# Kernel tuning notes

Hardware: AMD Instinct MI355X
Metric: run time of the kernel (lower is better)

The kernel has to match this reference:

```python
import jax, jax.numpy as jnp
import numpy as np

# dims (see shape_source)
N = 100000          # num_ent
E = 400000          # num edges
B = 2048            # batch of (sub, rel) queries
INIT_DIM = 100
UFD = 100           # user_fe_dim
ENT_DIM = INIT_DIM + 3 * UFD   # feature_method='concat' -> 400
H = 2               # attention heads
D = 64              # per-head dim
GCN = H * D         # gcn_dim = embed_dim = 128 (gcn_layer == 1)
NUM_REL = 50
NR2 = 2 * NUM_REL


def setup_inputs() -> dict:
    key = jax.random.key(0)
    ks = jax.random.split(key, 17)
    inp = {}
    # constructor / forward int tensors
    inp["edge_index"] = jax.random.randint(ks[0], (2, E), 0, N, dtype=jnp.int32)
    inp["edge_type"] = jax.random.randint(ks[1], (E,), 0, NR2, dtype=jnp.int32)
    inp["edge_type_p"] = jax.random.randint(ks[2], (E,), 0, NR2, dtype=jnp.int32)
    inp["ent_feature"] = jax.random.randint(ks[3], (N, 3), 0, 3, dtype=jnp.int32)
    inp["sub"] = jax.random.randint(ks[4], (B,), 0, N, dtype=jnp.int32)
    inp["rel"] = jax.random.randint(ks[5], (B,), 0, NR2, dtype=jnp.int32)
    inp["relp"] = jax.random.randint(ks[6], (B,), 0, NR2, dtype=jnp.int32)
    # learned parameters
    s = 0.02
    inp["id_embed"] = jax.random.normal(ks[7], (N, INIT_DIM), jnp.float32) * s
    inp["gender_tab"] = jax.random.normal(ks[8], (3, UFD), jnp.float32) * s
    inp["age_tab"] = jax.random.normal(ks[9], (9, UFD), jnp.float32) * s
    inp["level_tab"] = jax.random.normal(ks[10], (11, UFD), jnp.float32) * s
    inp["init_rel"] = jax.random.normal(ks[11], (NR2, ENT_DIM), jnp.float32) * s
    inp["W"] = jax.random.normal(ks[12], (ENT_DIM, H * D), jnp.float32) * 0.05
    inp["Wr"] = jax.random.normal(ks[13], (ENT_DIM, H * D), jnp.float32) * 0.05
    inp["att_src"] = jax.random.normal(ks[14], (H, D), jnp.float32) * 0.05
    inp["att_dst"] = jax.random.normal(ks[15], (H, D), jnp.float32) * 0.05
    inp["Wrel"] = jax.random.normal(ks[16], (ENT_DIM, GCN), jnp.float32) * 0.05
    return inp


def _segment_softmax(logits, seg, num_segments):
    # logits: [E, H], seg: [E] destination node ids
    m = jax.ops.segment_max(logits, seg, num_segments=num_segments)
    ex = jnp.exp(logits - m[seg])
    den = jax.ops.segment_sum(ex, seg, num_segments=num_segments)
    return ex / (den[seg] + 1e-16)


def _rghat_conv(x, rel_emb, edge_index, edge_type, W, Wr, att_src, att_dst, Wrel):
    # relational multi-head graph attention (RGHATConv)
    n = x.shape[0]
    h = (x @ W).reshape(n, H, D)                       # [N,H,D] projected nodes
    r_proj = (rel_emb @ Wr).reshape(-1, H, D)          # [R,H,D]
    src, dst = edge_index[0], edge_index[1]
    msg = h[src] + r_proj[edge_type]                   # [E,H,D] edge messages
    logits = jax.nn.leaky_relu(
        jnp.sum(msg * att_src, axis=-1) + jnp.sum(h[dst] * att_dst, axis=-1),
        negative_slope=0.2,
    )                                                  # [E,H]
    alpha = _segment_softmax(logits, dst, n)           # per-destination softmax
    out = jax.ops.segment_sum(alpha[..., None] * msg, dst, num_segments=n)
    out = jnp.tanh(out.reshape(n, H * D))              # [N,GCN]
    r_out = rel_emb @ Wrel                             # [R,GCN]
    return out, r_out


def reference(edge_index, edge_type, edge_type_p, ent_feature, sub, rel, relp,
              id_embed, gender_tab, age_tab, level_tab, init_rel,
              W, Wr, att_src, att_dst, Wrel):
    # feature_method == 'concat': gather per-node feature embeddings and concat
    x1 = gender_tab[ent_feature[:, 0]]
    x2 = age_tab[ent_feature[:, 1]]
    x3 = level_tab[ent_feature[:, 2]]
    init_embed = jnp.concatenate([id_embed, x1, x2, x3], axis=1)  # [N, ENT_DIM]
    # single conv layer (gcn_layer == 1); dropouts are identity in eval
    x, r = _rghat_conv(init_embed, init_rel, edge_index, edge_type,
                       W, Wr, att_src, att_dst, Wrel)
    sub_emb = x[sub]                                   # index_select gather
    # add_parent_rel == False -> r returned whole (relp unused)
    return (sub_emb, r, x)
```

## Files before the change

kernel.cpp:

```cpp
#include <hip/hip_runtime.h>
#include <hip/hip_bf16.h>
#include <hip/hip_fp16.h>

#define N_NODES 100000
#define E_EDGES 400000
#define B_SUB 2048
#define INIT_DIM 100
#define UFD 100
#define ENT_DIM 400
#define GCN 128
#define NR2 100
#define KPAD 416
#define NCH 13
#define CAP 64

typedef __attribute__((ext_vector_type(8))) short shortx8;
typedef __attribute__((ext_vector_type(4))) float floatx4;

#define OUT_R_OFF ((long)B_SUB * GCN)
#define OUT_X_OFF ((long)(B_SUB + NR2) * GCN)

__device__ __forceinline__ unsigned short f2b(float f) {
    unsigned u = __float_as_uint(f);
    u += 0x7fffu + ((u >> 16) & 1u);
    return (unsigned short)(u >> 16);
}
__device__ __forceinline__ unsigned pk2(float x, float y) {
    return (unsigned)f2b(x) | ((unsigned)f2b(y) << 16);
}
__device__ __forceinline__ float blo(unsigned u) { return __uint_as_float(u << 16); }
__device__ __forceinline__ float bhi(unsigned u) { return __uint_as_float(u & 0xFFFF0000u); }

__global__ void wt_kernel(const float* __restrict__ W, unsigned short* __restrict__ Wt,
                          int* __restrict__ cursor) {
    int idx = blockIdx.x * 256 + threadIdx.x;
    if (idx < GCN * KPAD) {
        int n = idx & 127, k = idx >> 7;
        unsigned short o = 0;
        if (k < ENT_DIM) o = f2b(W[(long)k * GCN + n]);
        Wt[(long)n * KPAD + k] = o;
    }
    if (idx < N_NODES) cursor[idx] = 0;
}

__global__ void rel_kernel(const float* __restrict__ init_rel, const float* __restrict__ Wr,
                           const float* __restrict__ Wrel, const float* __restrict__ att_src,
                           unsigned* __restrict__ rp_b, float* __restrict__ rproj_att,
                           float* __restrict__ out_r) {
    int rel = blockIdx.x;
    int tx = threadIdx.x;
    __shared__ float rl[ENT_DIM];
    __shared__ float accbuf[128];
    for (int k = tx; k < ENT_DIM; k += 128) rl[k] = init_rel[(long)rel * ENT_DIM + k];
    __syncthreads();
    float acc1 = 0.f, acc2 = 0.f;
    for (int k = 0; k < ENT_DIM; ++k) {
        float v = rl[k];
        acc1 += v * Wr[(long)k * GCN + tx];
        acc2 += v * Wrel[(long)k * GCN + tx];
    }
    out_r[rel * GCN + tx] = acc2;
    accbuf[tx] = acc1;
    int head = tx >> 6, d = tx & 63;
    float v = acc1 * att_src[head * 64 + d];
    for (int off = 32; off > 0; off >>= 1) v += __shfl_down(v, off, 64);
    if (d == 0) rproj_att[rel * 2 + head] = v;
    __syncthreads();
    if (tx < 64) rp_b[rel * 64 + tx] = pk2(accbuf[tx], accbuf[tx + 64]);
}

__global__ __launch_bounds__(512) void hgemm_kernel(
        const float* __restrict__ id_embed, const float* __restrict__ gtab,
        const float* __restrict__ atab, const float* __restrict__ ltab,
        const int* __restrict__ ent_feature, const unsigned short* __restrict__ Wt,
        const float* __restrict__ att_src, const float* __restrict__ att_dst,
        unsigned* __restrict__ h_b, float* __restrict__ hsrc_att, float* __restrict__ hdst_att) {
    __shared__ __align__(16) unsigned short Bs[GCN * KPAD];
    __shared__ float attS[GCN], attD[GCN];
    int t = threadIdx.x;
    if (t < GCN) { attS[t] = att_src[t]; attD[t] = att_dst[t]; }
    int w = t >> 6, lane = t & 63, quad = lane >> 4, l16 = lane & 15;
    int n0 = blockIdx.x * 128;
    int nrow = n0 + w * 16 + l16;
    int nclamp = nrow < N_NODES ? nrow : N_NODES - 1;
    int f0 = ent_feature[nclamp * 3];
    int f1 = ent_feature[nclamp * 3 + 1];
    int f2 = ent_feature[nclamp * 3 + 2];
    const float* pid = id_embed + (long)nclamp * INIT_DIM;
    const float* pg = gtab + f0 * UFD;
    const float* pa = atab + f1 * UFD;
    const float* pl = ltab + f2 * UFD;

    float4 va[NCH], vb[NCH];
#pragma unroll
    for (int ch = 0; ch < NCH; ++ch) {
        int kg = ch * 32 + quad * 8;
        const float* p0;
        if (kg < 100)      p0 = pid + kg;
        else if (kg < 200) p0 = pg + kg - 100;
        else if (kg < 300) p0 = pa + kg - 200;
        else if (kg < 400) p0 = pl + kg - 300;
        else               p0 = pid;
        va[ch] = *(const float4*)p0;
        int k4 = kg + 4;
        const float* p1;
        if (k4 < 100)      p1 = pid + k4;
        else if (k4 < 200) p1 = pg + k4 - 100;
        else if (k4 < 300) p1 = pa + k4 - 200;
        else if (k4 < 400) p1 = pl + k4 - 300;
        else               p1 = pid;
        vb[ch] = *(const float4*)p1;
    }

    {
        const char* gsrc = (const char*)Wt;
        char* lbase = (char*)Bs;
#pragma unroll
        for (int i = 0; i < NCH; ++i) {
            int off = i * 8192 + w * 1024;
            __builtin_amdgcn_global_load_lds(
                (const __attribute__((address_space(1))) unsigned int*)(gsrc + off + lane * 16),
                (__attribute__((address_space(3))) unsigned int*)(lbase + off), 16, 0, 0);
        }
    }

    shortx8 aF[NCH];
#pragma unroll
    for (int ch = 0; ch < NCH; ++ch) {
        uint4 u;
        u.x = pk2(va[ch].x, va[ch].y);
        u.y = pk2(va[ch].z, va[ch].w);
        u.z = pk2(vb[ch].x, vb[ch].y);
        u.w = pk2(vb[ch].z, vb[ch].w);
        aF[ch] = *(shortx8*)&u;
    }
    floatx4 acc[8];
#pragma unroll
    for (int c = 0; c < 8; ++c) acc[c] = (floatx4){0.f, 0.f, 0.f, 0.f};

    __syncthreads();

    const unsigned short* bp = &Bs[l16 * KPAD + quad * 8];
#pragma unroll
    for (int ch = 0; ch < NCH; ++ch) {
#pragma unroll
        for (int c = 0; c < 8; ++c) {
            shortx8 b = *(const shortx8*)&bp[c * 16 * KPAD + ch * 32];
            acc[c] = __builtin_amdgcn_mfma_f32_16x16x32_bf16(aF[ch], b, acc[c], 0, 0, 0);
        }
    }

    int baseRow = n0 + w * 16 + quad * 4;
#pragma unroll
    for (int i = 0; i < 4; ++i) {
        int node = baseRow + i;
        bool ok = node < N_NODES;
#pragma unroll
        for (int c = 0; c < 4; ++c)
            if (ok) h_b[(long)node * 64 + c * 16 + l16] = pk2(acc[c][i], acc[c + 4][i]);
        float s0 = 0.f, s1 = 0.f, d0 = 0.f, d1 = 0.f;
#pragma unroll
        for (int c = 0; c < 8; ++c) {
            float v = acc[c][i];
            float as_ = attS[c * 16 + l16], ad_ = attD[c * 16 + l16];
            if (c < 4) { s0 += v * as_; d0 += v * ad_; }
            else       { s1 += v * as_; d1 += v * ad_; }
        }
#pragma unroll
        for (int m = 1; m < 16; m <<= 1) {
            s0 += __shfl_xor(s0, m, 64);
            s1 += __shfl_xor(s1, m, 64);
            d0 += __shfl_xor(d0, m, 64);
            d1 += __shfl_xor(d1, m, 64);
        }
        if (ok && l16 == 0) {
            hsrc_att[node * 2] = s0; hsrc_att[node * 2 + 1] = s1;
            hdst_att[node * 2] = d0; hdst_att[node * 2 + 1] = d1;
        }
    }
}

__global__ void fill_kernel(const int* __restrict__ edge_index, const int* __restrict__ edge_type,
                            int* __restrict__ cursor,
                            const float2* __restrict__ hsrc2, const float2* __restrict__ rpa2,
                            const float2* __restrict__ hdst2,
                            uint2* __restrict__ ebuf) {
    int e = blockIdx.x * blockDim.x + threadIdx.x;
    if (e >= E_EDGES) return;
    int src = edge_index[e];
    int dst = edge_index[E_EDGES + e];
    int et = edge_type[e];
    float2 hs = hsrc2[src];
    float2 ra = rpa2[et];
    float2 hd = hdst2[dst];
    float x0 = hs.x + ra.x + hd.x;
    float x1 = hs.y + ra.y + hd.y;
    x0 = x0 > 0.f ? x0 : 0.2f * x0;
    x1 = x1 > 0.f ? x1 : 0.2f * x1;
    __half2 hh = __floats2half2_rn(__expf(x0), __expf(x1));
    union { __half2 h; unsigned u; } cv; cv.h = hh;
    int pos = atomicAdd(&cursor[dst], 1);
    if (pos < CAP)
        ebuf[(long)dst * CAP + pos] = make_uint2(((unsigned)et << 17) | (unsigned)src, cv.u);
}

__global__ __launch_bounds__(256) void agg_kernel(
        const int* __restrict__ cursor, const uint2* __restrict__ ebuf,
        const unsigned* __restrict__ h_b, const unsigned* __restrict__ rp_b,
        float* __restrict__ out_x) {
    int w = threadIdx.x >> 6, l = threadIdx.x & 63;
    int dst = blockIdx.x * 4 + w;
    int cnt = cursor[dst];
    if (cnt > CAP) cnt = CAP;
    const uint2* base = ebuf + (long)dst * CAP;
    float acc0 = 0.f, acc1 = 0.f, den0 = 0.f, den1 = 0.f;
    int j = 0;
    for (; j + 3 < cnt; j += 4) {
        uint2 v0 = base[j], v1 = base[j + 1], v2 = base[j + 2], v3 = base[j + 3];
        union { __half2 h; unsigned u; } c0, c1, c2, c3;
        c0.u = v0.y; c1.u = v1.y; c2.u = v2.y; c3.u = v3.y;
        float2 e0 = __half22float2(c0.h), e1 = __half22float2(c1.h);
        float2 e2 = __half22float2(c2.h), e3 = __half22float2(c3.h);
        unsigned hb0 = h_b[(long)(v0.x & 0x1FFFF) * 64 + l];
        unsigned hb1 = h_b[(long)(v1.x & 0x1FFFF) * 64 + l];
        unsigned hb2 = h_b[(long)(v2.x & 0x1FFFF) * 64 + l];
        unsigned hb3 = h_b[(long)(v3.x & 0x1FFFF) * 64 + l];
        unsigned rb0 = rp_b[(v0.x >> 17) * 64 + l];
        unsigned rb1 = rp_b[(v1.x >> 17) * 64 + l];
        unsigned rb2 = rp_b[(v2.x >> 17) * 64 + l];
        unsigned rb3 = rp_b[(v3.x >> 17) * 64 + l];
        acc0 += e0.x * (blo(hb0) + blo(rb0)) + e1.x * (blo(hb1) + blo(rb1))
              + e2.x * (blo(hb2) + blo(rb2)) + e3.x * (blo(hb3) + blo(rb3));
        acc1 += e0.y * (bhi(hb0) + bhi(rb0)) + e1.y * (bhi(hb1) + bhi(rb1))
              + e2.y * (bhi(hb2) + bhi(rb2)) + e3.y * (bhi(hb3) + bhi(rb3));
        den0 += e0.x + e1.x + e2.x + e3.x;
        den1 += e0.y + e1.y + e2.y + e3.y;
    }
    for (; j < cnt; ++j) {
        uint2 v0 = base[j];
        union { __half2 h; unsigned u; } c0; c0.u = v0.y;
        float2 e0 = __half22float2(c0.h);
        unsigned hb = h_b[(long)(v0.x & 0x1FFFF) * 64 + l];
        unsigned rb = rp_b[(v0.x >> 17) * 64 + l];
        acc0 += e0.x * (blo(hb) + blo(rb));
        acc1 += e0.y * (bhi(hb) + bhi(rb));
        den0 += e0.x;
        den1 += e0.y;
    }
    float i0 = 1.0f / (den0 + 1e-16f), i1 = 1.0f / (den1 + 1e-16f);
    __builtin_nontemporal_store(tanhf(acc0 * i0), &out_x[(long)dst * GCN + l]);
    __builtin_nontemporal_store(tanhf(acc1 * i1), &out_x[(long)dst * GCN + 64 + l]);
}

__global__ void gather_kernel(const int* __restrict__ sub, const float* __restrict__ out_x,
                              float* __restrict__ out_sub) {
    int idx = blockIdx.x * blockDim.x + threadIdx.x;
    if (idx >= B_SUB * GCN) return;
    int b = idx >> 7, d = idx & 127;
    out_sub[idx] = out_x[(long)sub[b] * GCN + d];
}

extern "C" void kernel_launch(void* const* d_in, const int* in_sizes, int n_in,
                              void* d_out, int out_size, void* d_ws, size_t ws_size,
                              hipStream_t stream) {
    const int* edge_index = (const int*)d_in[0];
    const int* edge_type  = (const int*)d_in[1];
    const int* ent_feature = (const int*)d_in[3];
    const int* sub = (const int*)d_in[4];
    const float* id_embed = (const float*)d_in[7];
    const float* gtab = (const float*)d_in[8];
    const float* atab = (const float*)d_in[9];
    const float* ltab = (const float*)d_in[10];
    const float* init_rel = (const float*)d_in[11];
    const float* W = (const float*)d_in[12];
    const float* Wr = (const float*)d_in[13];
    const float* att_src = (const float*)d_in[14];
    const float* att_dst = (const float*)d_in[15];
    const float* Wrel = (const float*)d_in[16];

    char* ws = (char*)d_ws;
    unsigned* h_b = (unsigned*)ws;                          ws += (long)N_NODES * 64 * 4;
    unsigned* rp_b = (unsigned*)ws;                         ws += (long)NR2 * 64 * 4;
    float* rproj_att = (float*)ws;                          ws += NR2 * 2 * 4;
    float* hsrc_att = (float*)ws;                           ws += (long)N_NODES * 2 * 4;
    float* hdst_att = (float*)ws;                           ws += (long)N_NODES * 2 * 4;
    unsigned short* Wt = (unsigned short*)ws;               ws += (long)GCN * KPAD * 2;
    int* cursor = (int*)ws;                                 ws += (long)N_NODES * 4;
    uint2* ebuf = (uint2*)ws;                               ws += (long)N_NODES * CAP * 8;

    float* out = (float*)d_out;
    float* out_sub = out;
    float* out_r = out + OUT_R_OFF;
    float* out_x = out + OUT_X_OFF;

    const int NB = (N_NODES + 255) / 256;

    wt_kernel<<<NB, 256, 0, stream>>>(W, Wt, cursor);
    rel_kernel<<<NR2, 128, 0, stream>>>(init_rel, Wr, Wrel, att_src, rp_b, rproj_att, out_r);
    hgemm_kernel<<<(N_NODES + 127) / 128, 512, 0, stream>>>(id_embed, gtab, atab, ltab,
                                                            ent_feature, Wt, att_src, att_dst,
                                                            h_b, hsrc_att, hdst_att);
    fill_kernel<<<(E_EDGES + 255) / 256, 256, 0, stream>>>(edge_index, edge_type, cursor,
                                                           (const float2*)hsrc_att,
                                                           (const float2*)rproj_att,
                                                           (const float2*)hdst_att, ebuf);
    agg_kernel<<<N_NODES / 4, 256, 0, stream>>>(cursor, ebuf, h_b, rp_b, out_x);
    gather_kernel<<<(B_SUB * GCN + 255) / 256, 256, 0, stream>>>(sub, out_x, out_sub);
}
```

Baseline: 246.9 us.

## Restructure node GEMM into register-tiled, double-buffered MFMA without LDS staging

The node projection GEMM moves from 512-thread blocks, where each wave did a 16x128 strip using a 106KB LDS copy of Wt, to 256-thread blocks. Each wave now computes a 64x64 register tile, reading Wt fragments directly from global/L2. A and B operand loads are double-buffered across K chunks to overlap with MFMA, and the fp32-to-bf16 packing uses the hardware v_cvt_pk_bf16_f32 instruction. The attention dot products are split across two column-half waves and combined through a small LDS buffer. This removes the large LDS footprint so more blocks can be resident, at the cost of more registers and repeated global reads of Wt.

New measurement: 263.2 us. 1.07x slower.

```diff
diff --git a/kernel.cpp b/kernel.cpp
--- a/kernel.cpp
+++ b/kernel.cpp
@@ -27,6 +27,11 @@
 }
 __device__ __forceinline__ unsigned pk2(float x, float y) {
     return (unsigned)f2b(x) | ((unsigned)f2b(y) << 16);
+}
+__device__ __forceinline__ unsigned cvtpk2(float x, float y) {
+    unsigned r;
+    asm("v_cvt_pk_bf16_f32 %0, %1, %2" : "=v"(r) : "v"(x), "v"(y));
+    return r;
 }
 __device__ __forceinline__ float blo(unsigned u) { return __uint_as_float(u << 16); }
 __device__ __forceinline__ float bhi(unsigned u) { return __uint_as_float(u & 0xFFFF0000u); }
@@ -69,115 +74,142 @@
     if (tx < 64) rp_b[rel * 64 + tx] = pk2(accbuf[tx], accbuf[tx + 64]);
 }
 
-__global__ __launch_bounds__(512) void hgemm_kernel(
+__device__ __forceinline__ float4 load_seg2(const float* __restrict__ id_embed,
+                                            const float* __restrict__ gtab,
+                                            const float* __restrict__ atab,
+                                            const float* __restrict__ ltab,
+                                            int ido, int go, int ao, int lo, int kg) {
+    const float* p;
+    if (kg < 100)      p = id_embed + ido + kg;
+    else if (kg < 200) p = gtab + go + (kg - 100);
+    else if (kg < 300) p = atab + ao + (kg - 200);
+    else if (kg < 400) p = ltab + lo + (kg - 300);
+    else               p = id_embed + ido;
+    return *(const float4*)p;
+}
+
+__global__ __launch_bounds__(256, 2) void hgemm_kernel(
         const float* __restrict__ id_embed, const float* __restrict__ gtab,
         const float* __restrict__ atab, const float* __restrict__ ltab,
         const int* __restrict__ ent_feature, const unsigned short* __restrict__ Wt,
         const float* __restrict__ att_src, const float* __restrict__ att_dst,
         unsigned* __restrict__ h_b, float* __restrict__ hsrc_att, float* __restrict__ hdst_att) {
-    __shared__ __align__(16) unsigned short Bs[GCN * KPAD];
-    __shared__ float attS[GCN], attD[GCN];
+    __shared__ float4 attp[2][128];
     int t = threadIdx.x;
-    if (t < GCN) { attS[t] = att_src[t]; attD[t] = att_dst[t]; }
     int w = t >> 6, lane = t & 63, quad = lane >> 4, l16 = lane & 15;
+    int rowhalf = w >> 1, hc = w & 1;
     int n0 = blockIdx.x * 128;
-    int nrow = n0 + w * 16 + l16;
-    int nclamp = nrow < N_NODES ? nrow : N_NODES - 1;
-    int f0 = ent_feature[nclamp * 3];
-    int f1 = ent_feature[nclamp * 3 + 1];
-    int f2 = ent_feature[nclamp * 3 + 2];
-    const float* pid = id_embed + (long)nclamp * INIT_DIM;
-    const float* pg = gtab + f0 * UFD;
-    const float* pa = atab + f1 * UFD;
-    const float* pl = ltab + f2 * UFD;
-
-    float4 va[NCH], vb[NCH];
-#pragma unroll
-    for (int ch = 0; ch < NCH; ++ch) {
-        int kg = ch * 32 + quad * 8;
-        const float* p0;
-        if (kg < 100)      p0 = pid + kg;
-        else if (kg < 200) p0 = pg + kg - 100;
-        else if (kg < 300) p0 = pa + kg - 200;
-        else if (kg < 400) p0 = pl + kg - 300;
-        else               p0 = pid;
-        va[ch] = *(const float4*)p0;
-        int k4 = kg + 4;
-        const float* p1;
-        if (k4 < 100)      p1 = pid + k4;
-        else if (k4 < 200) p1 = pg + k4 - 100;
-        else if (k4 < 300) p1 = pa + k4 - 200;
-        else if (k4 < 400) p1 = pl + k4 - 300;
-        else               p1 = pid;
-        vb[ch] = *(const float4*)p1;
-    }
-
-    {
-        const char* gsrc = (const char*)Wt;
-        char* lbase = (char*)Bs;
-#pragma unroll
-        for (int i = 0; i < NCH; ++i) {
-            int off = i * 8192 + w * 1024;
-            __builtin_amdgcn_global_load_lds(
-                (const __attribute__((address_space(1))) unsigned int*)(gsrc + off + lane * 16),
-                (__attribute__((address_space(3))) unsigned int*)(lbase + off), 16, 0, 0);
+    int rb = n0 + rowhalf * 64;
+
+    int ido[4], go[4], ao[4], lo[4];
+#pragma unroll
+    for (int rt = 0; rt < 4; ++rt) {
+        int nrow = rb + rt * 16 + l16;
+        int nc = nrow < N_NODES ? nrow : N_NODES - 1;
+        ido[rt] = nc * INIT_DIM;
+        go[rt] = ent_feature[nc * 3] * UFD;
+        ao[rt] = ent_feature[nc * 3 + 1] * UFD;
+        lo[rt] = ent_feature[nc * 3 + 2] * UFD;
+    }
+    const unsigned short* bp[4];
+#pragma unroll
+    for (int ct = 0; ct < 4; ++ct) {
+        int col = hc * 32 + (ct & 1) * 16 + (ct >> 1) * 64 + l16;
+        bp[ct] = Wt + (long)col * KPAD + quad * 8;
+    }
+
+    floatx4 acc[4][4];
+#pragma unroll
+    for (int rt = 0; rt < 4; ++rt)
+#pragma unroll
+        for (int ct = 0; ct < 4; ++ct) acc[rt][ct] = (floatx4){0.f, 0.f, 0.f, 0.f};
+
+    float4 a0[8], a1[8];
+    shortx8 b0[4], b1[4];
+
+#define LOADB(buf, ch_) {                                                   \
+    _Pragma("unroll") for (int ct = 0; ct < 4; ++ct)                        \
+        buf[ct] = *(const shortx8*)&bp[ct][(ch_) * 32]; }
+#define LOADA(buf, ch_) {                                                   \
+    int kg_ = (ch_) * 32 + quad * 8;                                        \
+    _Pragma("unroll") for (int rt = 0; rt < 4; ++rt) {                      \
+        buf[rt * 2]     = load_seg2(id_embed, gtab, atab, ltab,             \
+                                    ido[rt], go[rt], ao[rt], lo[rt], kg_);  \
+        buf[rt * 2 + 1] = load_seg2(id_embed, gtab, atab, ltab,             \
+                                    ido[rt], go[rt], ao[rt], lo[rt], kg_ + 4); \
+    } }
+#define COMP(abuf, bbuf) {                                                  \
+    _Pragma("unroll") for (int rt = 0; rt < 4; ++rt) {                      \
+        uint4 u_;                                                           \
+        u_.x = cvtpk2(abuf[rt * 2].x,     abuf[rt * 2].y);                  \
+        u_.y = cvtpk2(abuf[rt * 2].z,     abuf[rt * 2].w);                  \
+        u_.z = cvtpk2(abuf[rt * 2 + 1].x, abuf[rt * 2 + 1].y);              \
+        u_.w = cvtpk2(abuf[rt * 2 + 1].z, abuf[rt * 2 + 1].w);              \
+        shortx8 af_ = *(shortx8*)&u_;                                       \
+        _Pragma("unroll") for (int ct = 0; ct < 4; ++ct)                    \
+            acc[rt][ct] = __builtin_amdgcn_mfma_f32_16x16x32_bf16(          \
+                af_, bbuf[ct], acc[rt][ct], 0, 0, 0);                       \
+    } }
+
+    LOADB(b0, 0);
+    LOADA(a0, 0);
+#pragma unroll
+    for (int ch = 0; ch < 12; ch += 2) {
+        LOADB(b1, ch + 1);
+        LOADA(a1, ch + 1);
+        COMP(a0, b0);
+        LOADB(b0, ch + 2);
+        LOADA(a0, ch + 2);
+        COMP(a1, b1);
+    }
+    COMP(a0, b0);
+
+    float attS_r[4], attD_r[4];
+#pragma unroll
+    for (int ct = 0; ct < 4; ++ct) {
+        int col = hc * 32 + (ct & 1) * 16 + (ct >> 1) * 64 + l16;
+        attS_r[ct] = att_src[col];
+        attD_r[ct] = att_dst[col];
+    }
+#pragma unroll
+    for (int rt = 0; rt < 4; ++rt) {
+        int baseRow = rb + rt * 16 + quad * 4;
+#pragma unroll
+        for (int i = 0; i < 4; ++i) {
+            int node = baseRow + i;
+            bool ok = node < N_NODES;
+#pragma unroll
+            for (int p = 0; p < 2; ++p)
+                if (ok) h_b[(long)node * 64 + hc * 32 + p * 16 + l16] =
+                            pk2(acc[rt][p][i], acc[rt][p + 2][i]);
+            float s0 = acc[rt][0][i] * attS_r[0] + acc[rt][1][i] * attS_r[1];
+            float s1 = acc[rt][2][i] * attS_r[2] + acc[rt][3][i] * attS_r[3];
+            float d0 = acc[rt][0][i] * attD_r[0] + acc[rt][1][i] * attD_r[1];
+            float d1 = acc[rt][2][i] * attD_r[2] + acc[rt][3][i] * attD_r[3];
+#pragma unroll
+            for (int m = 1; m < 16; m <<= 1) {
+                s0 += __shfl_xor(s0, m, 64);
+                s1 += __shfl_xor(s1, m, 64);
+                d0 += __shfl_xor(d0, m, 64);
+                d1 += __shfl_xor(d1, m, 64);
+            }
+            if (l16 == 0)
+                attp[hc][rowhalf * 64 + rt * 16 + quad * 4 + i] = make_float4(s0, s1, d0, d1);
         }
     }
-
-    shortx8 aF[NCH];
-#pragma unroll
-    for (int ch = 0; ch < NCH; ++ch) {
-        uint4 u;
-        u.x = pk2(va[ch].x, va[ch].y);
-        u.y = pk2(va[ch].z, va[ch].w);
-        u.z = pk2(vb[ch].x, vb[ch].y);
-        u.w = pk2(vb[ch].z, vb[ch].w);
-        aF[ch] = *(shortx8*)&u;
-    }
-    floatx4 acc[8];
-#pragma unroll
-    for (int c = 0; c < 8; ++c) acc[c] = (floatx4){0.f, 0.f, 0.f, 0.f};
-
     __syncthreads();
-
-    const unsigned short* bp = &Bs[l16 * KPAD + quad * 8];
-#pragma unroll
-    for (int ch = 0; ch < NCH; ++ch) {
-#pragma unroll
-        for (int c = 0; c < 8; ++c) {
-            shortx8 b = *(const shortx8*)&bp[c * 16 * KPAD + ch * 32];
-            acc[c] = __builtin_amdgcn_mfma_f32_16x16x32_bf16(aF[ch], b, acc[c], 0, 0, 0);
+    if (hc == 0) {
+        int r = rowhalf * 64 + lane;
+        int node = n0 + r;
+        if (node < N_NODES) {
+            float4 pa_ = attp[0][r], pb_ = attp[1][r];
+            *(float2*)&hsrc_att[node * 2] = make_float2(pa_.x + pb_.x, pa_.y + pb_.y);
+            *(float2*)&hdst_att[node * 2] = make_float2(pa_.z + pb_.z, pa_.w + pb_.w);
         }
     }
-
-    int baseRow = n0 + w * 16 + quad * 4;
-#pragma unroll
-    for (int i = 0; i < 4; ++i) {
-        int node = baseRow + i;
-        bool ok = node < N_NODES;
-#pragma unroll
-        for (int c = 0; c < 4; ++c)
-            if (ok) h_b[(long)node * 64 + c * 16 + l16] = pk2(acc[c][i], acc[c + 4][i]);
-        float s0 = 0.f, s1 = 0.f, d0 = 0.f, d1 = 0.f;
-#pragma unroll
-        for (int c = 0; c < 8; ++c) {
-            float v = acc[c][i];
-            float as_ = attS[c * 16 + l16], ad_ = attD[c * 16 + l16];
-            if (c < 4) { s0 += v * as_; d0 += v * ad_; }
-            else       { s1 += v * as_; d1 += v * ad_; }
-        }
-#pragma unroll
-        for (int m = 1; m < 16; m <<= 1) {
-            s0 += __shfl_xor(s0, m, 64);
-            s1 += __shfl_xor(s1, m, 64);
-            d0 += __shfl_xor(d0, m, 64);
-            d1 += __shfl_xor(d1, m, 64);
-        }
-        if (ok && l16 == 0) {
-            hsrc_att[node * 2] = s0; hsrc_att[node * 2 + 1] = s1;
-            hdst_att[node * 2] = d0; hdst_att[node * 2 + 1] = d1;
-        }
-    }
+#undef LOADA
+#undef LOADB
+#undef COMP
 }
 
 __global__ void fill_kernel(const int* __restrict__ edge_index, const int* __restrict__ edge_type,
@@ -297,7 +329,7 @@
 
     wt_kernel<<<NB, 256, 0, stream>>>(W, Wt, cursor);
     rel_kernel<<<NR2, 128, 0, stream>>>(init_rel, Wr, Wrel, att_src, rp_b, rproj_att, out_r);
-    hgemm_kernel<<<(N_NODES + 127) / 128, 512, 0, stream>>>(id_embed, gtab, atab, ltab,
+    hgemm_kernel<<<(N_NODES + 127) / 128, 256, 0, stream>>>(id_embed, gtab, atab, ltab,
                                                             ent_feature, Wt, att_src, att_dst,
                                                             h_b, hsrc_att, hdst_att);
     fill_kernel<<<(E_EDGES + 255) / 256, 256, 0, stream>>>(edge_index, edge_type, cursor,
```
